# Optimization experiments

Hardware: AMD Instinct MI355X
Metric: run time of the kernel (lower is better)

## Reference

```python
import jax, jax.numpy as jnp
import numpy as np

N = 50000   # nodes
E = 1600000 # edges
K = 5       # Chebyshev order
F_IN, H1, H2, P = 32, 32, 16, 12


def setup_inputs() -> dict:
    key = jax.random.key(0)
    ks = jax.random.split(key, 16)
    x = jax.random.normal(ks[0], (N, F_IN), dtype=jnp.float32)
    edge_index = jax.random.randint(ks[1], (2, E), 0, N, dtype=jnp.int64)
    edge_weight = jax.random.uniform(ks[2], (E,), dtype=jnp.float32)
    s = 0.1
    # Cell 1: 3 gates (z, r, h), each with x-conv [K,F_IN,H1] and h-conv [K,H1,H1]
    Wx1 = jax.random.normal(ks[3], (3, K, F_IN, H1), dtype=jnp.float32) * s
    bx1 = jax.random.normal(ks[4], (3, H1), dtype=jnp.float32) * s
    Wh1 = jax.random.normal(ks[5], (3, K, H1, H1), dtype=jnp.float32) * s
    bh1 = jax.random.normal(ks[6], (3, H1), dtype=jnp.float32) * s
    # Cell 2
    Wx2 = jax.random.normal(ks[7], (3, K, H1, H2), dtype=jnp.float32) * s
    bx2 = jax.random.normal(ks[8], (3, H2), dtype=jnp.float32) * s
    Wh2 = jax.random.normal(ks[9], (3, K, H2, H2), dtype=jnp.float32) * s
    bh2 = jax.random.normal(ks[10], (3, H2), dtype=jnp.float32) * s
    # Output linear (torch convention: weight [out,in])
    Wl = jax.random.normal(ks[11], (P, H2), dtype=jnp.float32) * s
    bl = jax.random.normal(ks[12], (P,), dtype=jnp.float32) * s
    return dict(x=x, edge_index=edge_index, edge_weight=edge_weight,
                Wx1=Wx1, bx1=bx1, Wh1=Wh1, bh1=bh1,
                Wx2=Wx2, bx2=bx2, Wh2=Wh2, bh2=bh2, Wl=Wl, bl=bl)


def _cheb_norm(edge_index, edge_weight):
    # ChebConv 'sym' norm with lambda_max=2: L_hat off-diagonal = -D^-1/2 A D^-1/2,
    # diagonal cancels to 0 (get_laplacian +1 self loop, add_self_loops fill -1).
    row, col = edge_index[0], edge_index[1]
    deg = jax.ops.segment_sum(edge_weight, row, num_segments=N)
    dis = jnp.where(deg > 0, jax.lax.rsqrt(jnp.maximum(deg, 1e-30)), 0.0)
    return -dis[row] * edge_weight * dis[col]


def _gconv_gru_forward(x, edge_index, edge_weight, Wx1, bx1, Wh1, bh1,
                       Wx2, bx2, Wh2, bh2, Wl, bl):
    row, col = edge_index[0], edge_index[1]
    wn = _cheb_norm(edge_index, edge_weight)

    def spmm(v):  # (L_hat @ v): gather source rows, scatter-add to targets
        return jax.ops.segment_sum(v[row] * wn[:, None], col, num_segments=N)

    def cheb(v, W, b):  # W: [K, Fin, Fout]
        Tx0 = v
        out = Tx0 @ W[0]
        Tx1 = spmm(Tx0)
        out = out + Tx1 @ W[1]
        for k in range(2, K):
            Tx2 = 2.0 * spmm(Tx1) - Tx0
            out = out + Tx2 @ W[k]
            Tx0, Tx1 = Tx1, Tx2
        return out + b

    def gru_cell(v, H, Wx, bx, Wh, bh):
        Z = jax.nn.sigmoid(cheb(v, Wx[0], bx[0]) + cheb(H, Wh[0], bh[0]))
        R = jax.nn.sigmoid(cheb(v, Wx[1], bx[1]) + cheb(H, Wh[1], bh[1]))
        Ht = jnp.tanh(cheb(v, Wx[2], bx[2]) + cheb(H * R, Wh[2], bh[2]))
        return Z * H + (1.0 - Z) * Ht

    h = gru_cell(x, jnp.zeros((N, H1), x.dtype), Wx1, bx1, Wh1, bh1)
    h = jax.nn.relu(h)  # dropout is identity in eval mode
    h = gru_cell(h, jnp.zeros((N, H2), x.dtype), Wx2, bx2, Wh2, bh2)
    h = jax.nn.relu(h)
    return h @ Wl.T + bl


def reference(x, edge_index, edge_weight, Wx1, bx1, Wh1, bh1,
              Wx2, bx2, Wh2, bh2, Wl, bl):
    return _gconv_gru_forward(x, edge_index, edge_weight, Wx1, bx1, Wh1, bh1,
                              Wx2, bx2, Wh2, bh2, Wl, bl)
```

## Files before the change

### kernel.cpp

```cpp
#include <hip/hip_runtime.h>
#include <math.h>

#define NN 50000
#define NE 1600000
#define KORD 5
#define NB 196
#define QTR 12500
#define GE 782
#define MT 64
#define NBK 1563
#define NBP 1600
#define NCH 256
#define ECH (NE / NCH)
#define EC4 (NE / 64)
#define PADE 1800192

#define SCALE_W 2097152.0f
#define INV_SCALE_W (1.0f / 2097152.0f)
#define SCALE_D 4194304.0f
#define INV_SCALE_D (1.0f / 4194304.0f)

typedef _Float16 half8 __attribute__((ext_vector_type(8)));
typedef _Float16 half4v __attribute__((ext_vector_type(4)));
typedef float float4v __attribute__((ext_vector_type(4)));

__global__ __launch_bounds__(1024) void k_deg(const int* __restrict__ ei,
                                              const float* __restrict__ ew,
                                              int* __restrict__ deg_g) {
    __shared__ int h[QTR];
    int q = blockIdx.x >> 6, ch = blockIdx.x & 63;
    for (int i = threadIdx.x; i < QTR; i += 1024) h[i] = 0;
    __syncthreads();
    int base = ch * EC4, lo = q * QTR;
    for (int e = base + threadIdx.x; e < base + EC4; e += 1024) {
        int li = ei[e] - lo;
        if ((unsigned)li < (unsigned)QTR)
            atomicAdd(&h[li], __float2int_rn(ew[e] * SCALE_D));
    }
    __syncthreads();
    int* outp = deg_g + blockIdx.x * QTR;
    for (int i = threadIdx.x; i < QTR; i += 1024) outp[i] = h[i];
}

__global__ __launch_bounds__(256) void k_dis2(const int* __restrict__ deg_g,
                                              float* __restrict__ dis) {
    int n = blockIdx.x * 256 + threadIdx.x;
    if (n >= NN) return;
    int q = n / QTR, i = n % QTR;
    const int* p = deg_g + (q * 64) * QTR + i;
    int s = 0;
#pragma unroll
    for (int c = 0; c < 64; c++) s += p[c * QTR];
    float d = (float)s * INV_SCALE_D;
    dis[n] = s > 0 ? rsqrtf(fmaxf(d, 1e-30f)) : 0.f;
}

__global__ __launch_bounds__(1024) void k_bhist(const int* __restrict__ ei,
                                                int* __restrict__ bh) {
    __shared__ int hist[NBK];
    int ch = blockIdx.x;
    for (int i = threadIdx.x; i < NBK; i += 1024) hist[i] = 0;
    __syncthreads();
    const int* cols = ei + NE;
    int base = ch * ECH;
    for (int e = base + threadIdx.x; e < base + ECH; e += 1024)
        atomicAdd(&hist[cols[e] >> 5], 1);
    __syncthreads();
    int* outp = bh + ch * NBP;
    for (int b = threadIdx.x; b < NBK; b += 1024) outp[b] = hist[b];
}

__global__ __launch_bounds__(256) void k_btot(const int* __restrict__ bh,
                                              int* __restrict__ tot) {
    int b = blockIdx.x * 256 + threadIdx.x;
    if (b >= NBP) return;
    int s = 0;
    if (b < NBK) {
#pragma unroll 8
        for (int ch = 0; ch < NCH; ch++) s += bh[ch * NBP + b];
    }
    tot[b] = s;
}

__global__ __launch_bounds__(1024) void k_bscan1(const int* __restrict__ tot,
                                                 int* __restrict__ off_bk) {
    __shared__ int s[1024];
    int t = threadIdx.x;
    int a0 = (2 * t < NBP) ? tot[2 * t] : 0;
    int a1 = (2 * t + 1 < NBP) ? tot[2 * t + 1] : 0;
    int p0 = (a0 + 127) & ~127;
    int p1 = (a1 + 127) & ~127;
    s[t] = p0 + p1;
    __syncthreads();
    for (int d = 1; d < 1024; d <<= 1) {
        int u = (t >= d) ? s[t - d] : 0;
        __syncthreads();
        s[t] += u;
        __syncthreads();
    }
    int excl = (t == 0) ? 0 : s[t - 1];
    if (2 * t < NBK) off_bk[2 * t] = excl;
    if (2 * t + 1 < NBK) off_bk[2 * t + 1] = excl + p0;
    if (t == 1023) off_bk[NBK] = s[1023];
}

__global__ __launch_bounds__(256) void k_bcur(int* __restrict__ bh,
                                              const int* __restrict__ off_bk) {
    int b = blockIdx.x * 256 + threadIdx.x;
    if (b >= NBK) return;
    int run = off_bk[b];
    for (int ch = 0; ch < NCH; ch++) {
        int v = bh[ch * NBP + b];
        bh[ch * NBP + b] = run;
        run += v;
    }
}

__global__ __launch_bounds__(128) void k_pad(const int* __restrict__ off_bk,
                                             const int* __restrict__ tot,
                                             int2* __restrict__ edges) {
    int b = blockIdx.x;
    int start = off_bk[b] + tot[b];
    int end = off_bk[b + 1];
    for (int i = start + threadIdx.x; i < end; i += 128)
        edges[i] = make_int2(0, 0);
}

__global__ __launch_bounds__(1024) void k_cperm(const int* __restrict__ ei,
                                                const float* __restrict__ ew,
                                                const float* __restrict__ dis,
                                                const int* __restrict__ bh,
                                                int2* __restrict__ edges) {
    __shared__ int cur[NBK];
    int ch = blockIdx.x;
    const int* cp = bh + ch * NBP;
    for (int b = threadIdx.x; b < NBK; b += 1024) cur[b] = cp[b];
    __syncthreads();
    int base = ch * ECH;
    for (int e = base + threadIdx.x; e < base + ECH; e += 1024) {
        int r = ei[e], c = ei[NE + e];
        float w = -dis[r] * ew[e] * dis[c];
        int pos = atomicAdd(&cur[c >> 5], 1);
        int packed = (int)((unsigned)r | ((unsigned)(c & 31) << 16));
        edges[pos] = make_int2(packed, __float_as_int(w));
    }
}

#define SPMM_DS(C0, W0, G0, C1, W1, G1, C2, W2, G2, C3, W3, G3)      \
    {                                                                 \
        int* a0 = &acc[C0][sub * 4];                                  \
        int* a1 = &acc[C1][sub * 4];                                  \
        int* a2 = &acc[C2][sub * 4];                                  \
        int* a3 = &acc[C3][sub * 4];                                  \
        atomicAdd(a0 + 0, __float2int_rn(W0 * G0.x));                 \
        atomicAdd(a0 + 1, __float2int_rn(W0 * G0.y));                 \
        atomicAdd(a0 + 2, __float2int_rn(W0 * G0.z));                 \
        atomicAdd(a0 + 3, __float2int_rn(W0 * G0.w));                 \
        atomicAdd(a1 + 0, __float2int_rn(W1 * G1.x));                 \
        atomicAdd(a1 + 1, __float2int_rn(W1 * G1.y));                 \
        atomicAdd(a1 + 2, __float2int_rn(W1 * G1.z));                 \
        atomicAdd(a1 + 3, __float2int_rn(W1 * G1.w));                 \
        atomicAdd(a2 + 0, __float2int_rn(W2 * G2.x));                 \
        atomicAdd(a2 + 1, __float2int_rn(W2 * G2.y));                 \
        atomicAdd(a2 + 2, __float2int_rn(W2 * G2.z));                 \
        atomicAdd(a2 + 3, __float2int_rn(W2 * G2.w));                 \
        atomicAdd(a3 + 0, __float2int_rn(W3 * G3.x));                 \
        atomicAdd(a3 + 1, __float2int_rn(W3 * G3.y));                 \
        atomicAdd(a3 + 2, __float2int_rn(W3 * G3.z));                 \
        atomicAdd(a3 + 3, __float2int_rn(W3 * G3.w));                 \
    }

__global__ __launch_bounds__(256) void k_spmm(const int* __restrict__ off_bk,
                                              const int2* __restrict__ edges,
                                              const float* __restrict__ vin,
                                              const float* __restrict__ prev,
                                              float* __restrict__ vout,
                                              float scale) {
    __shared__ int acc[32][33];
    int b = blockIdx.x;
    for (int i = threadIdx.x; i < 32 * 33; i += 256) (&acc[0][0])[i] = 0;
    __syncthreads();
    int e0 = off_bk[b], e1 = off_bk[b + 1];
    int group = threadIdx.x >> 3, sub = threadIdx.x & 7;
    const float4* vin4 = (const float4*)vin;
    int i = e0 + group;
    if (i < e1) {
        int2 R0 = edges[i], R1 = edges[i + 32], R2 = edges[i + 64], R3 = edges[i + 96];
        float4 G0, G1, G2, G3;
        int C0 = 0, C1 = 0, C2 = 0, C3 = 0;
        float W0 = 0.f, W1 = 0.f, W2 = 0.f, W3 = 0.f;
        bool haveG = false;
        while (true) {
            int ni = i + 128;
            bool moreR = ni < e1;
            int2 N0, N1, N2, N3;
            if (moreR) {
                N0 = edges[ni]; N1 = edges[ni + 32];
                N2 = edges[ni + 64]; N3 = edges[ni + 96];
            }
            float4 g0 = vin4[((unsigned)R0.x & 0xffffu) * 8 + sub];
            float4 g1 = vin4[((unsigned)R1.x & 0xffffu) * 8 + sub];
            float4 g2 = vin4[((unsigned)R2.x & 0xffffu) * 8 + sub];
            float4 g3 = vin4[((unsigned)R3.x & 0xffffu) * 8 + sub];
            if (haveG) SPMM_DS(C0, W0, G0, C1, W1, G1, C2, W2, G2, C3, W3, G3);
            C0 = (unsigned)R0.x >> 16; C1 = (unsigned)R1.x >> 16;
            C2 = (unsigned)R2.x >> 16; C3 = (unsigned)R3.x >> 16;
            W0 = __int_as_float(R0.y) * SCALE_W;
            W1 = __int_as_float(R1.y) * SCALE_W;
            W2 = __int_as_float(R2.y) * SCALE_W;
            W3 = __int_as_float(R3.y) * SCALE_W;
            G0 = g0; G1 = g1; G2 = g2; G3 = g3;
            haveG = true;
            if (!moreR) break;
            R0 = N0; R1 = N1; R2 = N2; R3 = N3;
            i = ni;
        }
        SPMM_DS(C0, W0, G0, C1, W1, G1, C2, W2, G2, C3, W3, G3);
    }
    __syncthreads();
    float sf = scale * INV_SCALE_W;
    int base = b << 5;
    int nl = threadIdx.x >> 3, s4 = threadIdx.x & 7;
    int n = base + nl;
    if (n < NN) {
        const int* a = &acc[nl][s4 * 4];
        float4 o;
        if (prev) {
            float4 p = ((const float4*)prev)[n * 8 + s4];
            o = make_float4(fmaf(sf, (float)a[0], -p.x),
                            fmaf(sf, (float)a[1], -p.y),
                            fmaf(sf, (float)a[2], -p.z),
                            fmaf(sf, (float)a[3], -p.w));
        } else {
            o = make_float4(sf * (float)a[0], sf * (float)a[1],
                            sf * (float)a[2], sf * (float)a[3]);
        }
        ((float4*)vout)[n * 8 + s4] = o;
    }
}

__global__ __launch_bounds__(256) void k_epi1(
    const float* __restrict__ x, const float* __restrict__ t1,
    const float* __restrict__ t2, const float* __restrict__ t3,
    const float* __restrict__ t4, const float* __restrict__ Wx1,
    const float* __restrict__ bx1, const float* __restrict__ bh1,
    float* __restrict__ h) {
    __shared__ _Float16 T[5][MT][40];
    __shared__ _Float16 Wt[64][168];
    int n0 = blockIdx.x * MT;
    const float* bufs[5] = {x, t1, t2, t3, t4};
#pragma unroll
    for (int b = 0; b < 5; b++) {
        for (int idx = threadIdx.x; idx < MT * 8; idx += 256) {
            int r = idx >> 3, c4 = idx & 7;
            int rr = n0 + r; if (rr >= NN) rr = NN - 1;
            float4 v = *(const float4*)(bufs[b] + rr * 32 + c4 * 4);
            *(half4v*)&T[b][r][c4 * 4] =
                (half4v){(_Float16)v.x, (_Float16)v.y, (_Float16)v.z, (_Float16)v.w};
        }
    }
    const float* Wz = Wx1;
    const float* Wh = Wx1 + 2 * KORD * 32 * 32;
    for (int idx = threadIdx.x; idx < 160 * 64; idx += 256) {
        int k = idx >> 6, n = idx & 63;
        int b = k >> 5, i = k & 31;
        float w = (n < 32) ? Wz[b * 1024 + i * 32 + n]
                           : Wh[b * 1024 + i * 32 + (n - 32)];
        Wt[n][k] = (_Float16)w;
    }
    __syncthreads();
    int wave = threadIdx.x >> 6;
    int lane = threadIdx.x & 63;
    int lo = lane & 15, quad = lane >> 4;
    float4v acc[4];
#pragma unroll
    for (int t = 0; t < 4; t++) acc[t] = (float4v){0.f, 0.f, 0.f, 0.f};
#pragma unroll
    for (int b = 0; b < 5; b++) {
        half8 a = *(half8*)&T[b][wave * 16 + lo][quad * 8];
#pragma unroll
        for (int t = 0; t < 4; t++) {
            half8 bf = *(half8*)&Wt[t * 16 + lo][b * 32 + quad * 8];
            acc[t] = __builtin_amdgcn_mfma_f32_16x16x32_f16(a, bf, acc[t], 0, 0, 0);
        }
    }
    int nd_base = n0 + wave * 16 + quad * 4;
#pragma unroll
    for (int t = 0; t < 2; t++) {
        int j = t * 16 + lo;
        float bz = bx1[j] + bh1[j];
        float bhb = bx1[64 + j] + bh1[64 + j];
#pragma unroll
        for (int reg = 0; reg < 4; reg++) {
            int nd = nd_base + reg;
            if (nd < NN) {
                float zz = acc[t][reg] + bz;
                float hh = acc[t + 2][reg] + bhb;
                float z = 1.f / (1.f + __expf(-zz));
                float tt = __expf(-2.f * fabsf(hh));
                float ht = copysignf((1.f - tt) / (1.f + tt), hh);
                h[nd * 32 + j] = fmaxf((1.f - z) * ht, 0.f);
            }
        }
    }
}

__global__ __launch_bounds__(256) void k_epi2(
    const float* __restrict__ hin, const float* __restrict__ t1,
    const float* __restrict__ t2, const float* __restrict__ t3,
    const float* __restrict__ t4, const float* __restrict__ Wx2,
    const float* __restrict__ bx2, const float* __restrict__ bh2,
    const float* __restrict__ Wl, const float* __restrict__ bl,
    float* __restrict__ out) {
    __shared__ _Float16 T[5][MT][40];
    __shared__ _Float16 Wt[32][168];
    __shared__ float H2[MT][17];
    int n0 = blockIdx.x * MT;
    const float* bufs[5] = {hin, t1, t2, t3, t4};
#pragma unroll
    for (int b = 0; b < 5; b++) {
        for (int idx = threadIdx.x; idx < MT * 8; idx += 256) {
            int r = idx >> 3, c4 = idx & 7;
            int rr = n0 + r; if (rr >= NN) rr = NN - 1;
            float4 v = *(const float4*)(bufs[b] + rr * 32 + c4 * 4);
            *(half4v*)&T[b][r][c4 * 4] =
                (half4v){(_Float16)v.x, (_Float16)v.y, (_Float16)v.z, (_Float16)v.w};
        }
    }
    const float* Wz = Wx2;
    const float* Wh = Wx2 + 2 * KORD * 32 * 16;
    for (int idx = threadIdx.x; idx < 160 * 32; idx += 256) {
        int k = idx >> 5, n = idx & 31;
        int b = k >> 5, i = k & 31;
        float w = (n < 16) ? Wz[b * 512 + i * 16 + n]
                           : Wh[b * 512 + i * 16 + (n - 16)];
        Wt[n][k] = (_Float16)w;
    }
    __syncthreads();
    int wave = threadIdx.x >> 6;
    int lane = threadIdx.x & 63;
    int lo = lane & 15, quad = lane >> 4;
    float4v acc[2];
    acc[0] = (float4v){0.f, 0.f, 0.f, 0.f};
    acc[1] = (float4v){0.f, 0.f, 0.f, 0.f};
#pragma unroll
    for (int b = 0; b < 5; b++) {
        half8 a = *(half8*)&T[b][wave * 16 + lo][quad * 8];
#pragma unroll
        for (int t = 0; t < 2; t++) {
            half8 bf = *(half8*)&Wt[t * 16 + lo][b * 32 + quad * 8];
            acc[t] = __builtin_amdgcn_mfma_f32_16x16x32_f16(a, bf, acc[t], 0, 0, 0);
        }
    }
    {
        int j = lo;
        float bz = bx2[j] + bh2[j];
        float bhb = bx2[32 + j] + bh2[32 + j];
        int ndl_base = wave * 16 + quad * 4;
#pragma unroll
        for (int reg = 0; reg < 4; reg++) {
            float zz = acc[0][reg] + bz;
            float hh = acc[1][reg] + bhb;
            float z = 1.f / (1.f + __expf(-zz));
            float tt = __expf(-2.f * fabsf(hh));
            float ht = copysignf((1.f - tt) / (1.f + tt), hh);
            H2[ndl_base + reg][j] = fmaxf((1.f - z) * ht, 0.f);
        }
    }
    __syncthreads();
    for (int idx = threadIdx.x; idx < MT * 12; idx += 256) {
        int n = idx / 12, p = idx % 12;
        int gn = n0 + n;
        if (gn < NN) {
            float o = bl[p];
#pragma unroll
            for (int jj = 0; jj < 16; jj++) o = fmaf(H2[n][jj], Wl[p * 16 + jj], o);
            out[gn * 12 + p] = o;
        }
    }
}


extern "C" void kernel_launch(void* const* d_in, const int* in_sizes, int n_in,
                              void* d_out, int out_size, void* d_ws, size_t ws_size,
                              hipStream_t stream) {
    const float* x   = (const float*)d_in[0];
    const int*   ei  = (const int*)d_in[1];
    const float* ew  = (const float*)d_in[2];
    const float* Wx1 = (const float*)d_in[3];
    const float* bx1 = (const float*)d_in[4];
    const float* bh1 = (const float*)d_in[6];
    const float* Wx2 = (const float*)d_in[7];
    const float* bx2 = (const float*)d_in[8];
    const float* bh2 = (const float*)d_in[10];
    const float* Wl  = (const float*)d_in[11];
    const float* bl  = (const float*)d_in[12];
    float* out = (float*)d_out;

    float* ws     = (float*)d_ws;
    float* dis    = ws;
    int*   bh     = (int*)(ws + 50048);
    int*   tot    = bh + NCH * NBP;
    int*   off_bk = tot + NBP;
    int2*  edges  = (int2*)(off_bk + NBP);
    float* T1     = (float*)(edges + PADE);
    float* T2     = T1 + NN * 32;
    float* T3     = T2 + NN * 32;
    float* T4     = T3 + NN * 32;
    float* hb     = T4 + NN * 32;
    int*   deg_g  = (int*)T1;

    k_deg  <<<256, 1024, 0, stream>>>(ei, ew, deg_g);
    k_dis2 <<<NB, 256, 0, stream>>>(deg_g, dis);
    k_bhist<<<NCH, 1024, 0, stream>>>(ei, bh);
    k_btot <<<7, 256, 0, stream>>>(bh, tot);
    k_bscan1<<<1, 1024, 0, stream>>>(tot, off_bk);
    k_bcur <<<7, 256, 0, stream>>>(bh, off_bk);
    k_pad  <<<NBK, 128, 0, stream>>>(off_bk, tot, edges);
    k_cperm<<<NCH, 1024, 0, stream>>>(ei, ew, dis, bh, edges);

    k_spmm<<<NBK, 256, 0, stream>>>(off_bk, edges, x,  nullptr, T1, 1.f);
    k_spmm<<<NBK, 256, 0, stream>>>(off_bk, edges, T1, x,       T2, 2.f);
    k_spmm<<<NBK, 256, 0, stream>>>(off_bk, edges, T2, T1,      T3, 2.f);
    k_spmm<<<NBK, 256, 0, stream>>>(off_bk, edges, T3, T2,      T4, 2.f);
    k_epi1<<<GE, 256, 0, stream>>>(x, T1, T2, T3, T4, Wx1, bx1, bh1, hb);

    k_spmm<<<NBK, 256, 0, stream>>>(off_bk, edges, hb, nullptr, T1, 1.f);
    k_spmm<<<NBK, 256, 0, stream>>>(off_bk, edges, T1, hb,      T2, 2.f);
    k_spmm<<<NBK, 256, 0, stream>>>(off_bk, edges, T2, T1,      T3, 2.f);
    k_spmm<<<NBK, 256, 0, stream>>>(off_bk, edges, T3, T2,      T4, 2.f);
    k_epi2<<<GE, 256, 0, stream>>>(hb, T1, T2, T3, T4, Wx2, bx2, bh2, Wl, bl, out);
}
```

Baseline: 364.8 us.

## Gather SpMM inputs from fp16 copies of Chebyshev basis vectors

Each SpMM and epilogue stage now also writes an fp16 shadow of its output, and the SpMM gathers its source rows from that fp16 buffer, halving the bytes of the random gather traffic. The fp32 copies are kept for the recurrence term, and the last fp32 output (T4) is dropped. The epilogues read fp16 tiles directly instead of converting. A conversion kernel for x is added, the extra fp16 writes cost some bandwidth, and fp16 rounding of the recurrence inputs adds accuracy risk.

After: 345.9 us. 1.05x faster.

```diff
diff --git a/kernel.cpp b/kernel.cpp
--- a/kernel.cpp
+++ b/kernel.cpp
@@ -55,6 +55,16 @@
     dis[n] = s > 0 ? rsqrtf(fmaxf(d, 1e-30f)) : 0.f;
 }
 
+__global__ __launch_bounds__(256) void k_cvt(const float* __restrict__ x,
+                                             _Float16* __restrict__ x16) {
+    int i = blockIdx.x * 256 + threadIdx.x;
+    if (i < NN * 8) {
+        float4 v = ((const float4*)x)[i];
+        half4v h = {(_Float16)v.x, (_Float16)v.y, (_Float16)v.z, (_Float16)v.w};
+        *(half4v*)(x16 + i * 4) = h;
+    }
+}
+
 __global__ __launch_bounds__(1024) void k_bhist(const int* __restrict__ ei,
                                                 int* __restrict__ bh) {
     __shared__ int hist[NBK];
@@ -152,29 +162,32 @@
         int* a1 = &acc[C1][sub * 4];                                  \
         int* a2 = &acc[C2][sub * 4];                                  \
         int* a3 = &acc[C3][sub * 4];                                  \
-        atomicAdd(a0 + 0, __float2int_rn(W0 * G0.x));                 \
-        atomicAdd(a0 + 1, __float2int_rn(W0 * G0.y));                 \
-        atomicAdd(a0 + 2, __float2int_rn(W0 * G0.z));                 \
-        atomicAdd(a0 + 3, __float2int_rn(W0 * G0.w));                 \
-        atomicAdd(a1 + 0, __float2int_rn(W1 * G1.x));                 \
-        atomicAdd(a1 + 1, __float2int_rn(W1 * G1.y));                 \
-        atomicAdd(a1 + 2, __float2int_rn(W1 * G1.z));                 \
-        atomicAdd(a1 + 3, __float2int_rn(W1 * G1.w));                 \
-        atomicAdd(a2 + 0, __float2int_rn(W2 * G2.x));                 \
-        atomicAdd(a2 + 1, __float2int_rn(W2 * G2.y));                 \
-        atomicAdd(a2 + 2, __float2int_rn(W2 * G2.z));                 \
-        atomicAdd(a2 + 3, __float2int_rn(W2 * G2.w));                 \
-        atomicAdd(a3 + 0, __float2int_rn(W3 * G3.x));                 \
-        atomicAdd(a3 + 1, __float2int_rn(W3 * G3.y));                 \
-        atomicAdd(a3 + 2, __float2int_rn(W3 * G3.z));                 \
-        atomicAdd(a3 + 3, __float2int_rn(W3 * G3.w));                 \
-    }
+        atomicAdd(a0 + 0, __float2int_rn(W0 * (float)G0.x));          \
+        atomicAdd(a0 + 1, __float2int_rn(W0 * (float)G0.y));          \
+        atomicAdd(a0 + 2, __float2int_rn(W0 * (float)G0.z));          \
+        atomicAdd(a0 + 3, __float2int_rn(W0 * (float)G0.w));          \
+        atomicAdd(a1 + 0, __float2int_rn(W1 * (float)G1.x));          \
+        atomicAdd(a1 + 1, __float2int_rn(W1 * (float)G1.y));          \
+        atomicAdd(a1 + 2, __float2int_rn(W1 * (float)G1.z));          \
+        atomicAdd(a1 + 3, __float2int_rn(W1 * (float)G1.w));          \
+        atomicAdd(a2 + 0, __float2int_rn(W2 * (float)G2.x));          \
+        atomicAdd(a2 + 1, __float2int_rn(W2 * (float)G2.y));          \
+        atomicAdd(a2 + 2, __float2int_rn(W2 * (float)G2.z));          \
+        atomicAdd(a2 + 3, __float2int_rn(W2 * (float)G2.w));          \
+        atomicAdd(a3 + 0, __float2int_rn(W3 * (float)G3.x));          \
+        atomicAdd(a3 + 1, __float2int_rn(W3 * (float)G3.y));          \
+        atomicAdd(a3 + 2, __float2int_rn(W3 * (float)G3.z));          \
+        atomicAdd(a3 + 3, __float2int_rn(W3 * (float)G3.w));          \
+    }
+
+struct h4 { half4v v; };
 
 __global__ __launch_bounds__(256) void k_spmm(const int* __restrict__ off_bk,
                                               const int2* __restrict__ edges,
-                                              const float* __restrict__ vin,
+                                              const _Float16* __restrict__ vin16,
                                               const float* __restrict__ prev,
                                               float* __restrict__ vout,
+                                              _Float16* __restrict__ vout16,
                                               float scale) {
     __shared__ int acc[32][33];
     int b = blockIdx.x;
@@ -182,11 +195,11 @@
     __syncthreads();
     int e0 = off_bk[b], e1 = off_bk[b + 1];
     int group = threadIdx.x >> 3, sub = threadIdx.x & 7;
-    const float4* vin4 = (const float4*)vin;
+    const h4* vin4 = (const h4*)vin16;
     int i = e0 + group;
     if (i < e1) {
         int2 R0 = edges[i], R1 = edges[i + 32], R2 = edges[i + 64], R3 = edges[i + 96];
-        float4 G0, G1, G2, G3;
+        half4v G0, G1, G2, G3;
         int C0 = 0, C1 = 0, C2 = 0, C3 = 0;
         float W0 = 0.f, W1 = 0.f, W2 = 0.f, W3 = 0.f;
         bool haveG = false;
@@ -198,10 +211,10 @@
                 N0 = edges[ni]; N1 = edges[ni + 32];
                 N2 = edges[ni + 64]; N3 = edges[ni + 96];
             }
-            float4 g0 = vin4[((unsigned)R0.x & 0xffffu) * 8 + sub];
-            float4 g1 = vin4[((unsigned)R1.x & 0xffffu) * 8 + sub];
-            float4 g2 = vin4[((unsigned)R2.x & 0xffffu) * 8 + sub];
-            float4 g3 = vin4[((unsigned)R3.x & 0xffffu) * 8 + sub];
+            half4v g0 = vin4[((unsigned)R0.x & 0xffffu) * 8 + sub].v;
+            half4v g1 = vin4[((unsigned)R1.x & 0xffffu) * 8 + sub].v;
+            half4v g2 = vin4[((unsigned)R2.x & 0xffffu) * 8 + sub].v;
+            half4v g3 = vin4[((unsigned)R3.x & 0xffffu) * 8 + sub].v;
             if (haveG) SPMM_DS(C0, W0, G0, C1, W1, G1, C2, W2, G2, C3, W3, G3);
             C0 = (unsigned)R0.x >> 16; C1 = (unsigned)R1.x >> 16;
             C2 = (unsigned)R2.x >> 16; C3 = (unsigned)R3.x >> 16;
@@ -235,28 +248,29 @@
             o = make_float4(sf * (float)a[0], sf * (float)a[1],
                             sf * (float)a[2], sf * (float)a[3]);
         }
-        ((float4*)vout)[n * 8 + s4] = o;
+        if (vout) ((float4*)vout)[n * 8 + s4] = o;
+        half4v oh = {(_Float16)o.x, (_Float16)o.y, (_Float16)o.z, (_Float16)o.w};
+        *(half4v*)(vout16 + n * 32 + s4 * 4) = oh;
     }
 }
 
 __global__ __launch_bounds__(256) void k_epi1(
-    const float* __restrict__ x, const float* __restrict__ t1,
-    const float* __restrict__ t2, const float* __restrict__ t3,
-    const float* __restrict__ t4, const float* __restrict__ Wx1,
+    const _Float16* __restrict__ x16, const _Float16* __restrict__ t1,
+    const _Float16* __restrict__ t2, const _Float16* __restrict__ t3,
+    const _Float16* __restrict__ t4, const float* __restrict__ Wx1,
     const float* __restrict__ bx1, const float* __restrict__ bh1,
-    float* __restrict__ h) {
+    float* __restrict__ h, _Float16* __restrict__ h16) {
     __shared__ _Float16 T[5][MT][40];
     __shared__ _Float16 Wt[64][168];
     int n0 = blockIdx.x * MT;
-    const float* bufs[5] = {x, t1, t2, t3, t4};
+    const _Float16* bufs[5] = {x16, t1, t2, t3, t4};
 #pragma unroll
     for (int b = 0; b < 5; b++) {
-        for (int idx = threadIdx.x; idx < MT * 8; idx += 256) {
-            int r = idx >> 3, c4 = idx & 7;
+        for (int idx = threadIdx.x; idx < MT * 4; idx += 256) {
+            int r = idx >> 2, c8 = idx & 3;
             int rr = n0 + r; if (rr >= NN) rr = NN - 1;
-            float4 v = *(const float4*)(bufs[b] + rr * 32 + c4 * 4);
-            *(half4v*)&T[b][r][c4 * 4] =
-                (half4v){(_Float16)v.x, (_Float16)v.y, (_Float16)v.z, (_Float16)v.w};
+            half8 v = *(const half8*)(bufs[b] + rr * 32 + c8 * 8);
+            *(half8*)&T[b][r][c8 * 8] = v;
         }
     }
     const float* Wz = Wx1;
@@ -299,16 +313,18 @@
                 float z = 1.f / (1.f + __expf(-zz));
                 float tt = __expf(-2.f * fabsf(hh));
                 float ht = copysignf((1.f - tt) / (1.f + tt), hh);
-                h[nd * 32 + j] = fmaxf((1.f - z) * ht, 0.f);
+                float v = fmaxf((1.f - z) * ht, 0.f);
+                h[nd * 32 + j] = v;
+                h16[nd * 32 + j] = (_Float16)v;
             }
         }
     }
 }
 
 __global__ __launch_bounds__(256) void k_epi2(
-    const float* __restrict__ hin, const float* __restrict__ t1,
-    const float* __restrict__ t2, const float* __restrict__ t3,
-    const float* __restrict__ t4, const float* __restrict__ Wx2,
+    const _Float16* __restrict__ h16, const _Float16* __restrict__ t1,
+    const _Float16* __restrict__ t2, const _Float16* __restrict__ t3,
+    const _Float16* __restrict__ t4, const float* __restrict__ Wx2,
     const float* __restrict__ bx2, const float* __restrict__ bh2,
     const float* __restrict__ Wl, const float* __restrict__ bl,
     float* __restrict__ out) {
@@ -316,15 +332,14 @@
     __shared__ _Float16 Wt[32][168];
     __shared__ float H2[MT][17];
     int n0 = blockIdx.x * MT;
-    const float* bufs[5] = {hin, t1, t2, t3, t4};
+    const _Float16* bufs[5] = {h16, t1, t2, t3, t4};
 #pragma unroll
     for (int b = 0; b < 5; b++) {
-        for (int idx = threadIdx.x; idx < MT * 8; idx += 256) {
-            int r = idx >> 3, c4 = idx & 7;
+        for (int idx = threadIdx.x; idx < MT * 4; idx += 256) {
+            int r = idx >> 2, c8 = idx & 3;
             int rr = n0 + r; if (rr >= NN) rr = NN - 1;
-            float4 v = *(const float4*)(bufs[b] + rr * 32 + c4 * 4);
-            *(half4v*)&T[b][r][c4 * 4] =
-                (half4v){(_Float16)v.x, (_Float16)v.y, (_Float16)v.z, (_Float16)v.w};
+            half8 v = *(const half8*)(bufs[b] + rr * 32 + c8 * 8);
+            *(half8*)&T[b][r][c8 * 8] = v;
         }
     }
     const float* Wz = Wx2;
@@ -406,12 +421,18 @@
     float* T1     = (float*)(edges + PADE);
     float* T2     = T1 + NN * 32;
     float* T3     = T2 + NN * 32;
-    float* T4     = T3 + NN * 32;
-    float* hb     = T4 + NN * 32;
+    float* hb     = T3 + NN * 32;
+    _Float16* x16 = (_Float16*)(hb + NN * 32);
+    _Float16* t1h = x16 + NN * 32;
+    _Float16* t2h = t1h + NN * 32;
+    _Float16* t3h = t2h + NN * 32;
+    _Float16* t4h = t3h + NN * 32;
+    _Float16* hbh = t4h + NN * 32;
     int*   deg_g  = (int*)T1;
 
     k_deg  <<<256, 1024, 0, stream>>>(ei, ew, deg_g);
     k_dis2 <<<NB, 256, 0, stream>>>(deg_g, dis);
+    k_cvt  <<<(NN * 8 + 255) / 256, 256, 0, stream>>>(x, x16);
     k_bhist<<<NCH, 1024, 0, stream>>>(ei, bh);
     k_btot <<<7, 256, 0, stream>>>(bh, tot);
     k_bscan1<<<1, 1024, 0, stream>>>(tot, off_bk);
@@ -419,15 +440,15 @@
     k_pad  <<<NBK, 128, 0, stream>>>(off_bk, tot, edges);
     k_cperm<<<NCH, 1024, 0, stream>>>(ei, ew, dis, bh, edges);
 
-    k_spmm<<<NBK, 256, 0, stream>>>(off_bk, edges, x,  nullptr, T1, 1.f);
-    k_spmm<<<NBK, 256, 0, stream>>>(off_bk, edges, T1, x,       T2, 2.f);
-    k_spmm<<<NBK, 256, 0, stream>>>(off_bk, edges, T2, T1,      T3, 2.f);
-    k_spmm<<<NBK, 256, 0, stream>>>(off_bk, edges, T3, T2,      T4, 2.f);
-    k_epi1<<<GE, 256, 0, stream>>>(x, T1, T2, T3, T4, Wx1, bx1, bh1, hb);
-
-    k_spmm<<<NBK, 256, 0, stream>>>(off_bk, edges, hb, nullptr, T1, 1.f);
-    k_spmm<<<NBK, 256, 0, stream>>>(off_bk, edges, T1, hb,      T2, 2.f);
-    k_spmm<<<NBK, 256, 0, stream>>>(off_bk, edges, T2, T1,      T3, 2.f);
-    k_spmm<<<NBK, 256, 0, stream>>>(off_bk, edges, T3, T2,      T4, 2.f);
-    k_epi2<<<GE, 256, 0, stream>>>(hb, T1, T2, T3, T4, Wx2, bx2, bh2, Wl, bl, out);
-}
+    k_spmm<<<NBK, 256, 0, stream>>>(off_bk, edges, x16, nullptr, T1, t1h, 1.f);
+    k_spmm<<<NBK, 256, 0, stream>>>(off_bk, edges, t1h, x,      T2, t2h, 2.f);
+    k_spmm<<<NBK, 256, 0, stream>>>(off_bk, edges, t2h, T1,     T3, t3h, 2.f);
+    k_spmm<<<NBK, 256, 0, stream>>>(off_bk, edges, t3h, T2, nullptr, t4h, 2.f);
+    k_epi1<<<GE, 256, 0, stream>>>(x16, t1h, t2h, t3h, t4h, Wx1, bx1, bh1, hb, hbh);
+
+    k_spmm<<<NBK, 256, 0, stream>>>(off_bk, edges, hbh, nullptr, T1, t1h, 1.f);
+    k_spmm<<<NBK, 256, 0, stream>>>(off_bk, edges, t1h, hb,     T2, t2h, 2.f);
+    k_spmm<<<NBK, 256, 0, stream>>>(off_bk, edges, t2h, T1,     T3, t3h, 2.f);
+    k_spmm<<<NBK, 256, 0, stream>>>(off_bk, edges, t3h, T2, nullptr, t4h, 2.f);
+    k_epi2<<<GE, 256, 0, stream>>>(hbh, t1h, t2h, t3h, t4h, Wx2, bx2, bh2, Wl, bl, out);
+}
```
